# Performance work log

Hardware: AMD Instinct MI355X
Metric: run time of the kernel (lower is better)

Reference implementation:

```python
import jax, jax.numpy as jnp
import numpy as np

B, H0, W0, C = 8, 56, 56, 256
KC = VC = C
HID = 4 * C
NH = 8  # ChannelAttention default num_heads


def _ln(x, g, b, eps=1e-5):
    m = x.mean(-1, keepdims=True)
    v = jnp.var(x, axis=-1, keepdims=True)
    return (x - m) * jax.lax.rsqrt(v + eps) * g + b


def _dwconv(x, w, b, H, W):
    # x: [B, N, C] -> depthwise 3x3 on [B, C, H, W]
    Bn, N, Cc = x.shape
    t = x.transpose(0, 2, 1).reshape(Bn, Cc, H, W)
    y = jax.lax.conv_general_dilated(t, w, (1, 1), 'SAME', feature_group_count=Cc,
                                     dimension_numbers=('NCHW', 'OIHW', 'NCHW'))
    y = y + b[None, :, None, None]
    return y.reshape(Bn, Cc, H * W).transpose(0, 2, 1)


def _mixffn(x, H, W, w1, b1, dww, dwb, lg, lb, w2, b2):
    f = x @ w1.T + b1  # fc1(x), reused for the skip (torch computes it twice, same value)
    ax = jax.nn.gelu(_ln(_dwconv(f, dww, dwb, H, W) + f, lg, lb), approximate=False)
    return ax @ w2.T + b2


def _eff_attn(xn, kw, kb, qw, qb, vw, vb, rw, rb):
    # 1x1 convs == per-pixel linear; head_count=1
    k = jax.nn.softmax(xn @ kw.T + kb, axis=1)  # softmax over spatial N
    q = jax.nn.softmax(xn @ qw.T + qb, axis=2)  # softmax over key channels
    v = xn @ vw.T + vb
    ctx = jnp.einsum('bnk,bnv->bkv', k, v)      # [B, KC, VC]
    att = jnp.einsum('bkv,bnk->bnv', ctx, q)    # [B, N, VC]
    return att @ rw.T + rb


def _chan_attn(xn, temp, qkv_w, pw, pb):
    Bn, N, Cc = xn.shape
    d = Cc // NH
    qkv = (xn @ qkv_w.T).reshape(Bn, N, 3, NH, d).transpose(2, 0, 3, 4, 1)  # [3,B,h,d,N]
    q, k, v = qkv[0], qkv[1], qkv[2]
    q = q / jnp.maximum(jnp.linalg.norm(q, axis=-1, keepdims=True), 1e-12)
    k = k / jnp.maximum(jnp.linalg.norm(k, axis=-1, keepdims=True), 1e-12)
    attn = jax.nn.softmax(jnp.einsum('bhdn,bhen->bhde', q, k) * temp, axis=-1)  # [B,h,d,d]
    out = jnp.einsum('bhde,bhen->bhdn', attn, v).transpose(0, 3, 1, 2).reshape(Bn, N, Cc)
    return out @ pw.T + pb


def _forward(x, ln1g, ln1b, eakw, eakb, eaqw, eaqb, eavw, eavb, earw, earb,
             ln2g, ln2b, m1w1, m1b1, m1dww, m1dwb, m1lg, m1lb, m1w2, m1b2,
             ln3g, ln3b, catemp, caqkvw, capw, capb,
             ln4g, ln4b, m2w1, m2b1, m2dww, m2dwb, m2lg, m2lb, m2w2, m2b2, H, W):
    add1 = x + _eff_attn(_ln(x, ln1g, ln1b), eakw, eakb, eaqw, eaqb, eavw, eavb, earw, earb)
    add2 = add1 + _mixffn(_ln(add1, ln2g, ln2b), H, W, m1w1, m1b1, m1dww, m1dwb, m1lg, m1lb, m1w2, m1b2)
    add3 = add2 + _chan_attn(_ln(add2, ln3g, ln3b), catemp, caqkvw, capw, capb)
    return add3 + _mixffn(_ln(add3, ln4g, ln4b), H, W, m2w1, m2b1, m2dww, m2dwb, m2lg, m2lb, m2w2, m2b2)


def setup_inputs() -> dict:
    key = jax.random.key(0)
    ks = jax.random.split(key, 16)
    s = 0.02
    rn = lambda k, shape: jax.random.normal(k, shape, jnp.float32) * s
    f32 = jnp.float32
    return {
        'x': jax.random.normal(ks[0], (B, H0 * W0, C), f32),
        'H': H0, 'W': W0,
        'ln1g': jnp.ones(C, f32), 'ln1b': jnp.zeros(C, f32),
        'eakw': rn(ks[1], (KC, C)), 'eakb': jnp.zeros(KC, f32),
        'eaqw': rn(ks[2], (KC, C)), 'eaqb': jnp.zeros(KC, f32),
        'eavw': rn(ks[3], (VC, C)), 'eavb': jnp.zeros(VC, f32),
        'earw': rn(ks[4], (C, VC)), 'earb': jnp.zeros(C, f32),
        'ln2g': jnp.ones(C, f32), 'ln2b': jnp.zeros(C, f32),
        'm1w1': rn(ks[5], (HID, C)), 'm1b1': jnp.zeros(HID, f32),
        'm1dww': rn(ks[6], (HID, 1, 3, 3)), 'm1dwb': jnp.zeros(HID, f32),
        'm1lg': jnp.ones(HID, f32), 'm1lb': jnp.zeros(HID, f32),
        'm1w2': rn(ks[7], (C, HID)), 'm1b2': jnp.zeros(C, f32),
        'ln3g': jnp.ones(C, f32), 'ln3b': jnp.zeros(C, f32),
        'catemp': jnp.ones((NH, 1, 1), f32),
        'caqkvw': rn(ks[8], (3 * C, C)),
        'capw': rn(ks[9], (C, C)), 'capb': jnp.zeros(C, f32),
        'ln4g': jnp.ones(C, f32), 'ln4b': jnp.zeros(C, f32),
        'm2w1': rn(ks[10], (HID, C)), 'm2b1': jnp.zeros(HID, f32),
        'm2dww': rn(ks[11], (HID, 1, 3, 3)), 'm2dwb': jnp.zeros(HID, f32),
        'm2lg': jnp.ones(HID, f32), 'm2lb': jnp.zeros(HID, f32),
        'm2w2': rn(ks[12], (C, HID)), 'm2b2': jnp.zeros(C, f32),
    }


def reference(x, H, W, ln1g, ln1b, eakw, eakb, eaqw, eaqb, eavw, eavb, earw, earb,
              ln2g, ln2b, m1w1, m1b1, m1dww, m1dwb, m1lg, m1lb, m1w2, m1b2,
              ln3g, ln3b, catemp, caqkvw, capw, capb,
              ln4g, ln4b, m2w1, m2b1, m2dww, m2dwb, m2lg, m2lb, m2w2, m2b2):
    return _forward(x, ln1g, ln1b, eakw, eakb, eaqw, eaqb, eavw, eavb, earw, earb,
                    ln2g, ln2b, m1w1, m1b1, m1dww, m1dwb, m1lg, m1lb, m1w2, m1b2,
                    ln3g, ln3b, catemp, caqkvw, capw, capb,
                    ln4g, ln4b, m2w1, m2b1, m2dww, m2dwb, m2lg, m2lb, m2w2, m2b2, H, W)
```

## Files before the change

### kernel.cpp

```cpp
#include <hip/hip_runtime.h>
#include <hip/hip_bf16.h>

typedef __hip_bfloat16 bf16;
typedef __attribute__((ext_vector_type(8))) short short8;
typedef __attribute__((ext_vector_type(4))) float floatx4;

#define DI __device__ __forceinline__

DI float ldf(const float* p, long long i){ return p[i]; }
DI float ldf(const bf16* p, long long i){ return __bfloat162float(p[i]); }

DI unsigned short bfbits(float f){
    bf16 h = __float2bfloat16(f);
    return *reinterpret_cast<unsigned short*>(&h);
}
DI float bu(unsigned short u){
    union { unsigned int i; float f; } x; x.i = ((unsigned int)u) << 16; return x.f;
}

DI float gelu_exact(float x){
    float z = fabsf(x) * 0.70710678118654752f;
    float t = __builtin_amdgcn_rcpf(fmaf(0.3275911f, z, 1.f));
    float p = t * fmaf(t, fmaf(t, fmaf(t, fmaf(t, 1.061405429f, -1.453152027f),
                    1.421413741f), -0.284496736f), 0.254829592f);
    float e = __expf(-z*z);
    float er = fmaf(-p, e, 1.f);
    er = copysignf(er, x);
    return 0.5f * x * (1.f + er);
}

DI void gload16(const void* g, void* l){
    __builtin_amdgcn_global_load_lds(
        (const __attribute__((address_space(1))) unsigned int*)g,
        (__attribute__((address_space(3))) unsigned int*)l,
        16, 0, 0);
}

static constexpr int BATCH = 8;
static constexpr int HH = 56, WW = 56;
static constexpr int NPOS = HH * WW;
static constexpr int CDIM = 256;
static constexpr int HIDD = 1024;
static constexpr int MTOT = BATCH * NPOS;
static constexpr int NCHUNK = 49;
static constexpr int LP = 40;
static constexpr int TNS = 7;

struct WArgs {
    const float* src[10];
    bf16* dst[10];
    int n[10];
};
__global__ __launch_bounds__(256) void wcvt_kernel(WArgs a){
    int wid = blockIdx.y;
    int i = (blockIdx.x*256 + threadIdx.x) * 8;
    if (i >= a.n[wid]) return;
    const float* s = a.src[wid] + i;
    float4 f0 = *(const float4*)(s);
    float4 f1 = *(const float4*)(s + 4);
    union { uint4 u; unsigned short us[8]; } p;
    p.us[0]=bfbits(f0.x); p.us[1]=bfbits(f0.y); p.us[2]=bfbits(f0.z); p.us[3]=bfbits(f0.w);
    p.us[4]=bfbits(f1.x); p.us[5]=bfbits(f1.y); p.us[6]=bfbits(f1.z); p.us[7]=bfbits(f1.w);
    *(uint4*)(a.dst[wid] + i) = p.u;
}

__global__ __launch_bounds__(256) void wtrans_kernel(const float* __restrict__ w1, const float* __restrict__ w2,
                                                     float* __restrict__ t1, float* __restrict__ t2){
    int i = blockIdx.x*256 + threadIdx.x;
    const float* w = blockIdx.y ? w2 : w1;
    float* t = blockIdx.y ? t2 : t1;
    int tap = i >> 10, c = i & 1023;
    t[i] = w[c*9 + tap];
}

template<typename TC>
__global__ __launch_bounds__(256) void mfma_gemm(
    const bf16* __restrict__ A, const bf16* __restrict__ Bw,
    const float* __restrict__ bias, const float* __restrict__ addend,
    TC* __restrict__ C, int M, int N, int K, int lda,
    long long strA, long long strB, long long strC, long long strAdd)
{
    __shared__ __align__(16) float smemf[4608];
    short* As = (short*)smemf;
    short* Bs = (short*)smemf + 4096;
    int tid = threadIdx.x;
    int bz = blockIdx.z;
    A  += (long long)bz * strA;
    Bw += (long long)bz * strB;
    C  += (long long)bz * strC;
    if (addend) addend += (long long)bz * strAdd;

    int gx = gridDim.x;
    int nwg = gx * gridDim.y;
    int bidl = blockIdx.y * gx + blockIdx.x;
    int qq = nwg >> 3, rr = nwg & 7;
    int xcd = bidl & 7, ixx = bidl >> 3;
    int tile = (xcd < rr) ? (xcd*(qq+1) + ixx) : (rr*(qq+1) + (xcd-rr)*qq + ixx);
    int n0 = (tile % gx) * 128, m0 = (tile / gx) * 128;

    int w = tid >> 6, lane = tid & 63, lm = lane & 15, quad = lane >> 4;
    int mw = (w >> 1) * 64, nw = (w & 1) * 64;

    int c0 = w*128 + lane, c1 = c0 + 64;
    int ar0 = c0 >> 2, ac0 = (c0 & 3) ^ (ar0 & 3);
    int ar1 = c1 >> 2, ac1 = (c1 & 3) ^ (ar1 & 3);
    int rgA0 = m0 + ar0; if (rgA0 > M-1) rgA0 = M-1;
    int rgA1 = m0 + ar1; if (rgA1 > M-1) rgA1 = M-1;
    short* aL0 = &As[(2*w+0)*512];
    short* aL1 = &As[(2*w+1)*512];
    short* bL0 = &Bs[(2*w+0)*512];
    short* bL1 = &Bs[(2*w+1)*512];
    const bf16* Arow0 = A + (long long)rgA0*lda + ac0*8;
    const bf16* Arow1 = A + (long long)rgA1*lda + ac1*8;
    const bf16* Brow0 = Bw + (long long)(n0+ar0)*K + ac0*8;
    const bf16* Brow1 = Bw + (long long)(n0+ar1)*K + ac1*8;

    floatx4 z = {0.f, 0.f, 0.f, 0.f};
    floatx4 acc[4][4];
    #pragma unroll
    for (int mi = 0; mi < 4; mi++)
        #pragma unroll
        for (int ni = 0; ni < 4; ni++) acc[mi][ni] = z;

    int sq = quad ^ (lm & 3);

    for (int k0 = 0; k0 < K; k0 += 32){
        gload16(Arow0 + k0, aL0);
        gload16(Arow1 + k0, aL1);
        gload16(Brow0 + k0, bL0);
        gload16(Brow1 + k0, bL1);
        __syncthreads();
        short8 af[4], bfr[4];
        #pragma unroll
        for (int mi = 0; mi < 4; mi++)
            af[mi] = *(const short8*)&As[(((mw + mi*16 + lm)<<2) + sq)*8];
        #pragma unroll
        for (int ni = 0; ni < 4; ni++)
            bfr[ni] = *(const short8*)&Bs[(((nw + ni*16 + lm)<<2) + sq)*8];
        #pragma unroll
        for (int mi = 0; mi < 4; mi++)
            #pragma unroll
            for (int ni = 0; ni < 4; ni++)
                acc[mi][ni] = __builtin_amdgcn_mfma_f32_16x16x32_bf16(af[mi], bfr[ni], acc[mi][ni], 0, 0, 0);
        __syncthreads();
    }

    float bvv[4];
    #pragma unroll
    for (int ni = 0; ni < 4; ni++)
        bvv[ni] = bias ? bias[n0 + nw + ni*16 + lm] : 0.f;
    float* esc = smemf + w*1088;
    int rl0 = lane >> 3;
    #pragma unroll
    for (int mi = 0; mi < 4; mi++){
        #pragma unroll
        for (int ni = 0; ni < 4; ni++)
            #pragma unroll
            for (int r = 0; r < 4; r++)
                esc[(quad*4 + r)*68 + ni*16 + lm] = acc[mi][ni][r] + bvv[ni];
        #pragma unroll
        for (int p = 0; p < 2; p++){
            int rloc = p*8 + rl0;
            int rg = m0 + mw + mi*16 + rloc;
            if (rg < M){
                if constexpr (sizeof(TC) == 2){
                    int cl = (lane & 7) * 8;
                    float4 u0 = *(const float4*)&esc[rloc*68 + cl];
                    float4 u1 = *(const float4*)&esc[rloc*68 + cl + 4];
                    if (addend){
                        long long ai = (long long)rg*N + (n0 + nw + cl);
                        float4 a0 = *(const float4*)(addend + ai);
                        float4 a1 = *(const float4*)(addend + ai + 4);
                        u0.x+=a0.x; u0.y+=a0.y; u0.z+=a0.z; u0.w+=a0.w;
                        u1.x+=a1.x; u1.y+=a1.y; u1.z+=a1.z; u1.w+=a1.w;
                    }
                    union { uint4 u; unsigned short us[8]; } pk;
                    pk.us[0]=bfbits(u0.x); pk.us[1]=bfbits(u0.y); pk.us[2]=bfbits(u0.z); pk.us[3]=bfbits(u0.w);
                    pk.us[4]=bfbits(u1.x); pk.us[5]=bfbits(u1.y); pk.us[6]=bfbits(u1.z); pk.us[7]=bfbits(u1.w);
                    *(uint4*)(C + (long long)rg*N + (n0 + nw + cl)) = pk.u;
                } else {
                    int cl4 = (lane & 7) * 4;
                    long long co = (long long)rg*N + (n0 + nw);
                    float4 u0 = *(const float4*)&esc[rloc*68 + cl4];
                    float4 u1 = *(const float4*)&esc[rloc*68 + 32 + cl4];
                    if (addend){
                        float4 a0 = *(const float4*)(addend + co + cl4);
                        float4 a1 = *(const float4*)(addend + co + 32 + cl4);
                        u0.x+=a0.x; u0.y+=a0.y; u0.z+=a0.z; u0.w+=a0.w;
                        u1.x+=a1.x; u1.y+=a1.y; u1.z+=a1.z; u1.w+=a1.w;
                    }
                    *(float4*)(C + co + cl4) = u0;
                    *(float4*)(C + co + 32 + cl4) = u1;
                }
            }
        }
    }
}

__global__ __launch_bounds__(256) void gemm_tn_mfma(const bf16* __restrict__ V, const bf16* __restrict__ Kb,
                                                    float* __restrict__ part){
    __shared__ short As[128*LP];
    __shared__ short Bs[128*LP];
    int tid = threadIdx.x;
    int bz = blockIdx.z;
    int b = bz / TNS, s = bz % TNS;
    const bf16* Vb = V  + (long long)b*NPOS*CDIM;
    const bf16* Kc = Kb + (long long)b*NPOS*CDIM;
    int m0 = blockIdx.y * 128, n0 = blockIdx.x * 128;
    int w = tid >> 6, lane = tid & 63, lm = lane & 15, quad = lane >> 4;
    int mw = (w >> 1) * 64, nw = (w & 1) * 64;

    floatx4 z = {0.f,0.f,0.f,0.f};
    floatx4 acc[4][4];
    #pragma unroll
    for (int mi = 0; mi < 4; mi++)
        #pragma unroll
        for (int ni = 0; ni < 4; ni++) acc[mi][ni] = z;

    int r = tid & 31, cgrp = tid >> 5;

    for (int step = 0; step < 448/32; step++){
        int nb = s*448 + step*32;
        #pragma unroll
        for (int cc = 0; cc < 2; cc++){
            int ch = cgrp*8 + cc*64;
            short8 va = *(const short8*)(Vb + (long long)(nb + r)*CDIM + m0 + ch);
            short8 ka = *(const short8*)(Kc + (long long)(nb + r)*CDIM + n0 + ch);
            #pragma unroll
            for (int i = 0; i < 8; i++){
                As[(ch+i)*LP + r] = va[i];
                Bs[(ch+i)*LP + r] = ka[i];
            }
        }
        __syncthreads();
        short8 af[4], bfr[4];
        #pragma unroll
        for (int mi = 0; mi < 4; mi++)
            af[mi] = *(const short8*)&As[(mw + mi*16 + lm)*LP + quad*8];
        #pragma unroll
        for (int ni = 0; ni < 4; ni++)
            bfr[ni] = *(const short8*)&Bs[(nw + ni*16 + lm)*LP + quad*8];
        #pragma unroll
        for (int mi = 0; mi < 4; mi++)
            #pragma unroll
            for (int ni = 0; ni < 4; ni++)
                acc[mi][ni] = __builtin_amdgcn_mfma_f32_16x16x32_bf16(af[mi], bfr[ni], acc[mi][ni], 0, 0, 0);
        __syncthreads();
    }

    float* pb = part + (long long)bz * CDIM * CDIM;
    #pragma unroll
    for (int ni = 0; ni < 4; ni++){
        int cg = n0 + nw + ni*16 + lm;
        #pragma unroll
        for (int mi = 0; mi < 4; mi++){
            #pragma unroll
            for (int rr = 0; rr < 4; rr++){
                int rg = m0 + mw + mi*16 + quad*4 + rr;
                pb[(long long)rg*CDIM + cg] = acc[mi][ni][rr];
            }
        }
    }
}

__global__ __launch_bounds__(256) void ctx_reduce(const float* __restrict__ part, bf16* __restrict__ ctxb){
    long long idx = (long long)blockIdx.x*256 + threadIdx.x;
    int b = (int)(idx >> 16);
    int rem = (int)(idx & 65535);
    float s = 0.f;
    #pragma unroll
    for (int sp = 0; sp < TNS; sp++)
        s += part[((long long)(b*TNS+sp) << 16) + rem];
    ctxb[idx] = __float2bfloat16(s);
}

DI void st4o(float* p, long long i, float a, float b, float c, float d){
    float4 v = make_float4(a,b,c,d); *(float4*)(p + i) = v;
}
DI void st4o(bf16* p, long long i, float a, float b, float c, float d){
    union { unsigned long long u; unsigned short us[4]; } pk;
    pk.us[0]=bfbits(a); pk.us[1]=bfbits(b); pk.us[2]=bfbits(c); pk.us[3]=bfbits(d);
    *(unsigned long long*)(p + i) = pk.u;
}
template<typename TOUT>
__global__ __launch_bounds__(256) void ln4_kernel(const float* __restrict__ x, const float* __restrict__ g,
                                                  const float* __restrict__ b, TOUT* __restrict__ y){
    int wv = threadIdx.x >> 6, lane = threadIdx.x & 63;
    long long row = (long long)blockIdx.x*4 + wv;
    float4 v = *(const float4*)(x + row*256 + lane*4);
    float s  = v.x + v.y + v.z + v.w;
    float ss = v.x*v.x + v.y*v.y + v.z*v.z + v.w*v.w;
    #pragma unroll
    for (int off = 32; off > 0; off >>= 1){
        s  += __shfl_down(s,  off);
        ss += __shfl_down(ss, off);
    }
    s = __shfl(s, 0); ss = __shfl(ss, 0);
    float mean = s * (1.f/256.f);
    float var  = ss * (1.f/256.f) - mean*mean;
    float inv  = rsqrtf(var + 1e-5f);
    float4 gv = *(const float4*)(g + lane*4);
    float4 bv = *(const float4*)(b + lane*4);
    st4o(y, row*256 + lane*4,
         (v.x-mean)*inv*gv.x + bv.x, (v.y-mean)*inv*gv.y + bv.y,
         (v.z-mean)*inv*gv.z + bv.z, (v.w-mean)*inv*gv.w + bv.w);
}

__global__ __launch_bounds__(256) void colsm_p1(const float* __restrict__ x, float* __restrict__ lmax, float* __restrict__ lsum){
    int b = blockIdx.x / NCHUNK, ch = blockIdx.x % NCHUNK;
    int c = threadIdx.x;
    const float* base = x + ((long long)b*NPOS + ch*64)*512 + c;
    float m = -1e30f;
    for (int r = 0; r < 64; r++) m = fmaxf(m, base[(long long)r*512]);
    float s = 0.f;
    for (int r = 0; r < 64; r++) s += expf(base[(long long)r*512] - m);
    lmax[(long long)blockIdx.x*CDIM + c] = m;
    lsum[(long long)blockIdx.x*CDIM + c] = s;
}
__global__ __launch_bounds__(256) void colsm_p2(const float* __restrict__ lmax, const float* __restrict__ lsum,
                                                float* __restrict__ gmax, float* __restrict__ ginv){
    int b = blockIdx.x; int c = threadIdx.x;
    float g = -1e30f;
    for (int ch = 0; ch < NCHUNK; ch++) g = fmaxf(g, lmax[((long long)b*NCHUNK+ch)*CDIM + c]);
    float s = 0.f;
    for (int ch = 0; ch < NCHUNK; ch++)
        s += lsum[((long long)b*NCHUNK+ch)*CDIM + c] * expf(lmax[((long long)b*NCHUNK+ch)*CDIM + c] - g);
    gmax[b*CDIM + c] = g; ginv[b*CDIM + c] = 1.f / s;
}
__global__ __launch_bounds__(256) void colsm_p3(const float* __restrict__ x, bf16* __restrict__ y,
                                                const float* __restrict__ gmax, const float* __restrict__ ginv){
    long long idx = (long long)blockIdx.x*256 + threadIdx.x;
    int c = (int)(idx & 255);
    long long row = idx >> 8;
    int b = (int)(row / NPOS);
    y[idx] = __float2bfloat16(expf(x[row*512 + c] - gmax[b*CDIM + c]) * ginv[b*CDIM + c]);
}

__global__ __launch_bounds__(256) void rowsm4b_kernel(const float* __restrict__ x, const float* __restrict__ bias,
                                                      bf16* __restrict__ y){
    int wv = threadIdx.x >> 6, lane = threadIdx.x & 63;
    long long row = (long long)blockIdx.x*4 + wv;
    float4 v = *(const float4*)(x + row*512 + 256 + lane*4);
    float4 bb = *(const float4*)(bias + lane*4);
    v.x += bb.x; v.y += bb.y; v.z += bb.z; v.w += bb.w;
    float m = fmaxf(fmaxf(v.x, v.y), fmaxf(v.z, v.w));
    #pragma unroll
    for (int off = 32; off > 0; off >>= 1) m = fmaxf(m, __shfl_down(m, off));
    m = __shfl(m, 0);
    float e0 = expf(v.x - m), e1 = expf(v.y - m), e2 = expf(v.z - m), e3 = expf(v.w - m);
    float s = e0 + e1 + e2 + e3;
    #pragma unroll
    for (int off = 32; off > 0; off >>= 1) s += __shfl_down(s, off);
    s = __shfl(s, 0);
    float inv = 1.f / s;
    st4o(y, row*256 + lane*4, e0*inv, e1*inv, e2*inv, e3*inv);
}

__global__ __launch_bounds__(256) void dwconv_ln_gelu_kernel(const bf16* __restrict__ f, const float* __restrict__ wT,
        const float* __restrict__ db, const float* __restrict__ lg, const float* __restrict__ lb, bf16* __restrict__ out){
    __shared__ short Ls[18*1024];
    __shared__ float r1[2][2][128], r2[2][2][128];
    int tid = threadIdx.x;
    int b = blockIdx.x & 7;
    int rem = blockIdx.x >> 3;
    int h = rem / 14, w0 = (rem % 14) * 4;
    const bf16* fb = f + (long long)b * NPOS * HIDD;

    #pragma unroll
    for (int j = 0; j < 9; j++){
        int idx = j*256 + tid;
        int rc = idx >> 7, chunk = idx & 127;
        int row = rc / 6, col = rc % 6;
        int hy = h - 1 + row, wx = w0 - 1 + col;
        uint4 v = {0,0,0,0};
        if (hy >= 0 && hy < HH && wx >= 0 && wx < WW)
            v = *(const uint4*)(fb + (long long)(hy*WW + wx)*HIDD + chunk*8);
        *(uint4*)&Ls[rc*1024 + chunk*8] = v;
    }
    __syncthreads();

    int ph = tid >> 7, ct = tid & 127;
    int c0 = ct * 8;
    float sv[2][8];
    {
        float4 d0 = *(const float4*)(db + c0);
        float4 d1 = *(const float4*)(db + c0 + 4);
        #pragma unroll
        for (int pp = 0; pp < 2; pp++){
            sv[pp][0]=d0.x; sv[pp][1]=d0.y; sv[pp][2]=d0.z; sv[pp][3]=d0.w;
            sv[pp][4]=d1.x; sv[pp][5]=d1.y; sv[pp][6]=d1.z; sv[pp][7]=d1.w;
        }
    }
    #pragma unroll
    for (int tap = 0; tap < 9; tap++){
        int ky = tap / 3, kx = tap % 3;
        float4 w0v = *(const float4*)(wT + tap*1024 + c0);
        float4 w1v = *(const float4*)(wT + tap*1024 + c0 + 4);
        float wv[8] = {w0v.x,w0v.y,w0v.z,w0v.w,w1v.x,w1v.y,w1v.z,w1v.w};
        #pragma unroll
        for (int pp = 0; pp < 2; pp++){
            int pos_local = 2*ph + pp;
            short8 val = *(const short8*)&Ls[(ky*6 + pos_local + kx)*1024 + c0];
            #pragma unroll
            for (int i = 0; i < 8; i++){
                float fv = bu((unsigned short)val[i]);
                sv[pp][i] += fv * wv[i];
                if (tap == 4) sv[pp][i] += fv;
            }
        }
    }
    #pragma unroll
    for (int pp = 0; pp < 2; pp++){
        float s = 0.f, ss = 0.f;
        #pragma unroll
        for (int i = 0; i < 8; i++){ s += sv[pp][i]; ss += sv[pp][i]*sv[pp][i]; }
        r1[ph][pp][ct] = s; r2[ph][pp][ct] = ss;
    }
    __syncthreads();
    for (int st = 64; st > 0; st >>= 1){
        if (ct < st){
            #pragma unroll
            for (int pp = 0; pp < 2; pp++){
                r1[ph][pp][ct] += r1[ph][pp][ct+st];
                r2[ph][pp][ct] += r2[ph][pp][ct+st];
            }
        }
        __syncthreads();
    }
    float4 g0 = *(const float4*)(lg + c0), g1 = *(const float4*)(lg + c0 + 4);
    float4 b0 = *(const float4*)(lb + c0), b1 = *(const float4*)(lb + c0 + 4);
    float gg[8] = {g0.x,g0.y,g0.z,g0.w,g1.x,g1.y,g1.z,g1.w};
    float bb[8] = {b0.x,b0.y,b0.z,b0.w,b1.x,b1.y,b1.z,b1.w};
    #pragma unroll
    for (int pp = 0; pp < 2; pp++){
        int pos_local = 2*ph + pp;
        long long n = (long long)b*NPOS + h*WW + (w0 + pos_local);
        float mean = r1[ph][pp][0] * (1.f/HIDD);
        float var  = r2[ph][pp][0] * (1.f/HIDD) - mean*mean;
        float inv  = rsqrtf(var + 1e-5f);
        union { uint4 u; unsigned short us[8]; } ov;
        #pragma unroll
        for (int i = 0; i < 8; i++){
            float o = (sv[pp][i]-mean)*inv*gg[i] + bb[i];
            ov.us[i] = bfbits(gelu_exact(o));
        }
        *(uint4*)(out + n*HIDD + c0) = ov.u;
    }
}

__global__ __launch_bounds__(256) void ssq_p1(const bf16* __restrict__ qkv, float* __restrict__ lss){
    __shared__ float red[4][64][8];
    int b = blockIdx.x / NCHUNK, ch = blockIdx.x % NCHUNK;
    int tid = threadIdx.x;
    int col = (tid & 63) * 8;
    int rg = tid >> 6;
    float s[8] = {0,0,0,0,0,0,0,0};
    for (int r = rg*16; r < rg*16 + 16; r++){
        long long row = (long long)(b*NPOS + ch*64 + r);
        union { uint4 u; unsigned short us[8]; } v;
        v.u = *(const uint4*)(qkv + row*768 + col);
        #pragma unroll
        for (int i = 0; i < 8; i++){ float f = bu(v.us[i]); s[i] += f*f; }
    }
    #pragma unroll
    for (int i = 0; i < 8; i++) red[rg][tid & 63][i] = s[i];
    __syncthreads();
    if (tid < 64){
        #pragma unroll
        for (int i = 0; i < 8; i++){
            float t = red[0][tid][i] + red[1][tid][i] + red[2][tid][i] + red[3][tid][i];
            lss[(long long)blockIdx.x*512 + tid*8 + i] = t;
        }
    }
}
__global__ __launch_bounds__(256) void ssq_p2(const float* __restrict__ lss, float* __restrict__ invn){
    int b = blockIdx.x; int c = blockIdx.y*256 + threadIdx.x;
    float s = 0.f;
    for (int ch = 0; ch < NCHUNK; ch++) s += lss[((long long)b*NCHUNK+ch)*512 + c];
    invn[b*512 + c] = 1.f / fmaxf(sqrtf(s), 1e-12f);
}

__global__ __launch_bounds__(256) void chanattn_qk_part(const bf16* __restrict__ qkv, const float* __restrict__ invn,
                                                        float* __restrict__ part){
    __shared__ float qs[64][36];
    __shared__ float ks[64][36];
    int bz = blockIdx.x;
    int bh = bz / TNS, s = bz % TNS;
    int b = bh >> 3, hh = bh & 7;
    int tid = threadIdx.x;
    int d = tid >> 3, e0 = (tid & 7) * 4;
    int sr = tid >> 2, sc8 = (tid & 3) * 8;
    float invq[8], invk[8];
    {
        float4 a0 = *(const float4*)(invn + b*512 + hh*32 + sc8);
        float4 a1 = *(const float4*)(invn + b*512 + hh*32 + sc8 + 4);
        float4 b0 = *(const float4*)(invn + b*512 + 256 + hh*32 + sc8);
        float4 b1 = *(const float4*)(invn + b*512 + 256 + hh*32 + sc8 + 4);
        invq[0]=a0.x; invq[1]=a0.y; invq[2]=a0.z; invq[3]=a0.w;
        invq[4]=a1.x; invq[5]=a1.y; invq[6]=a1.z; invq[7]=a1.w;
        invk[0]=b0.x; invk[1]=b0.y; invk[2]=b0.z; invk[3]=b0.w;
        invk[4]=b1.x; invk[5]=b1.y; invk[6]=b1.z; invk[7]=b1.w;
    }
    float acc[4] = {0.f,0.f,0.f,0.f};
    for (int it = 0; it < 7; it++){
        int n0 = s*448 + it*64;
        {
            long long rowb = (long long)(b*NPOS + n0 + sr) * 768;
            union { uint4 u; unsigned short us[8]; } qv, kv;
            qv.u = *(const uint4*)(qkv + rowb + hh*32 + sc8);
            kv.u = *(const uint4*)(qkv + rowb + 256 + hh*32 + sc8);
            #pragma unroll
            for (int i = 0; i < 8; i++){
                qs[sr][sc8+i] = bu(qv.us[i]) * invq[i];
                ks[sr][sc8+i] = bu(kv.us[i]) * invk[i];
            }
        }
        __syncthreads();
        #pragma unroll 4
        for (int r = 0; r < 64; r++){
            float qv = qs[r][d];
            #pragma unroll
            for (int j = 0; j < 4; j++) acc[j] += qv * ks[r][e0+j];
        }
        __syncthreads();
    }
    #pragma unroll
    for (int j = 0; j < 4; j++)
        part[(long long)bz*1024 + d*32 + e0 + j] = acc[j];
}
__global__ __launch_bounds__(256) void chanattn_qk_fin(const float* __restrict__ part, const float* __restrict__ temp,
                                                       float* __restrict__ attn){
    __shared__ float att_s[32][33];
    int bh = blockIdx.x;
    int hh = bh & 7;
    int tid = threadIdx.x;
    int d = tid >> 3, e0 = (tid & 7) * 4;
    float t = temp[hh];
    #pragma unroll
    for (int j = 0; j < 4; j++){
        float s = 0.f;
        for (int sp = 0; sp < TNS; sp++)
            s += part[((long long)bh*TNS + sp)*1024 + d*32 + e0 + j];
        att_s[d][e0+j] = s * t;
    }
    __syncthreads();
    if (tid < 32){
        float m = -1e30f;
        for (int e = 0; e < 32; e++) m = fmaxf(m, att_s[tid][e]);
        float s = 0.f;
        for (int e = 0; e < 32; e++){ float ev = expf(att_s[tid][e] - m); att_s[tid][e] = ev; s += ev; }
        float inv = 1.f / s;
        for (int e = 0; e < 32; e++) att_s[tid][e] *= inv;
    }
    __syncthreads();
    #pragma unroll
    for (int j = 0; j < 4; j++)
        attn[(long long)bh*1024 + d*32 + e0 + j] = att_s[d][e0+j];
}

__global__ __launch_bounds__(256) void wcomb_kernel(const float* __restrict__ capw, const float* __restrict__ attn,
                                                    bf16* __restrict__ Wb){
    __shared__ float at_s[8192];
    int b = blockIdx.x, og = blockIdx.y;
    int tid = threadIdx.x;
    #pragma unroll
    for (int j = 0; j < 8; j++)
        *(float4*)&at_s[tid*32 + j*4] = *(const float4*)(attn + (long long)b*8192 + tid*32 + j*4);
    __syncthreads();
    int o = og*32 + (tid & 31);
    int h = tid >> 5;
    float acc[32];
    #pragma unroll
    for (int e = 0; e < 32; e++) acc[e] = 0.f;
    for (int d = 0; d < 32; d++){
        float w = capw[(long long)o*256 + h*32 + d];
        const float* ar = &at_s[h*1024 + d*32];
        #pragma unroll
        for (int eq = 0; eq < 8; eq++){
            float4 av = *(const float4*)(ar + eq*4);
            acc[eq*4+0] += w*av.x; acc[eq*4+1] += w*av.y;
            acc[eq*4+2] += w*av.z; acc[eq*4+3] += w*av.w;
        }
    }
    bf16* dst = Wb + (long long)b*65536 + (long long)o*256 + h*32;
    #pragma unroll
    for (int eq = 0; eq < 4; eq++){
        union { uint4 u; unsigned short us[8]; } p;
        #pragma unroll
        for (int i = 0; i < 8; i++) p.us[i] = bfbits(acc[eq*8+i]);
        *(uint4*)(dst + eq*8) = p.u;
    }
}

extern "C" void kernel_launch(void* const* d_in, const int* in_sizes, int n_in,
                              void* d_out, int out_size, void* d_ws, size_t ws_size,
                              hipStream_t stream){
    const float* x     = (const float*)d_in[0];
    const float* ln1g  = (const float*)d_in[3];
    const float* ln1b  = (const float*)d_in[4];
    const float* eakw  = (const float*)d_in[5];
    const float* eaqw  = (const float*)d_in[7];
    const float* eaqb  = (const float*)d_in[8];
    const float* eavw  = (const float*)d_in[9];
    const float* eavb  = (const float*)d_in[10];
    const float* earw  = (const float*)d_in[11];
    const float* earb  = (const float*)d_in[12];
    const float* ln2g  = (const float*)d_in[13];
    const float* ln2b  = (const float*)d_in[14];
    const float* m1w1  = (const float*)d_in[15];
    const float* m1b1  = (const float*)d_in[16];
    const float* m1dww = (const float*)d_in[17];
    const float* m1dwb = (const float*)d_in[18];
    const float* m1lg  = (const float*)d_in[19];
    const float* m1lb  = (const float*)d_in[20];
    const float* m1w2  = (const float*)d_in[21];
    const float* m1b2  = (const float*)d_in[22];
    const float* ln3g  = (const float*)d_in[23];
    const float* ln3b  = (const float*)d_in[24];
    const float* catemp= (const float*)d_in[25];
    const float* caqkvw= (const float*)d_in[26];
    const float* capw  = (const float*)d_in[27];
    const float* capb  = (const float*)d_in[28];
    const float* ln4g  = (const float*)d_in[29];
    const float* ln4b  = (const float*)d_in[30];
    const float* m2w1  = (const float*)d_in[31];
    const float* m2b1  = (const float*)d_in[32];
    const float* m2dww = (const float*)d_in[33];
    const float* m2dwb = (const float*)d_in[34];
    const float* m2lg  = (const float*)d_in[35];
    const float* m2lb  = (const float*)d_in[36];
    const float* m2w2  = (const float*)d_in[37];
    const float* m2b2  = (const float*)d_in[38];

    char* base = (char*)d_ws;
    auto alloc = [&](size_t nbytes){ char* p = base; base += (nbytes + 255) & ~(size_t)255; return p; };
    constexpr size_t SZ = (size_t)MTOT*CDIM*4;
    float* R  = (float*)alloc(SZ);
    float* A0 = (float*)alloc(SZ);
    float* A1 = (float*)alloc(SZ);
    float* B0 = (float*)alloc(SZ);
    float* B1 = (float*)alloc(SZ);
    bf16* A0b  = (bf16*)A0;
    bf16* kb   = (bf16*)A0;
    bf16* qb   = A0b + (size_t)MTOT*CDIM;
    bf16* vb   = (bf16*)A1;
    float* KQ  = B0;
    bf16* attb = (bf16*)B0;
    bf16* l2b  = (bf16*)A1;
    bf16* F    = (bf16*)B0;
    bf16* G    = (bf16*)A0;
    bf16* l3b  = (bf16*)B0;
    bf16* Qb   = (bf16*)A0;
    bf16* l4b  = (bf16*)A0;
    bf16* ctxb = (bf16*)alloc((size_t)BATCH*CDIM*CDIM*2);
    float* lmax = (float*)alloc((size_t)BATCH*NCHUNK*CDIM*4);
    float* lsum = (float*)alloc((size_t)BATCH*NCHUNK*CDIM*4);
    float* gmax = (float*)alloc((size_t)BATCH*CDIM*4);
    float* ginv = (float*)alloc((size_t)BATCH*CDIM*4);
    float* lss  = (float*)alloc((size_t)BATCH*NCHUNK*512*4);
    float* invn = (float*)alloc((size_t)BATCH*512*4);
    float* attnb= (float*)alloc((size_t)BATCH*8*32*32*4);
    float* ptn  = (float*)alloc((size_t)BATCH*TNS*CDIM*CDIM*4);
    float* pqk  = (float*)alloc((size_t)BATCH*8*TNS*1024*4);
    bf16* wbuf  = (bf16*)alloc((size_t)1572864*2);
    float* wT1  = (float*)alloc((size_t)9216*4);
    float* wT2  = (float*)alloc((size_t)9216*4);
    bf16* Wcb   = (bf16*)alloc((size_t)BATCH*CDIM*CDIM*2);

    bf16* kqw_b    = wbuf;
    bf16* eavw_b   = wbuf + 131072;
    bf16* earw_b   = wbuf + 196608;
    bf16* m1w1_b   = wbuf + 262144;
    bf16* m1w2_b   = wbuf + 524288;
    bf16* caqkvw_b = wbuf + 786432;
    bf16* m2w1_b   = wbuf + 1048576;
    bf16* m2w2_b   = wbuf + 1310720;

    dim3 blk(256);
    constexpr int MB = MTOT/128;
    long long sA1 = (long long)NPOS*CDIM;
    long long sB1 = (long long)CDIM*CDIM;

    {
        WArgs wa;
        const float* srcs[10] = {eakw, eaqw, eavw, earw, m1w1, m1w2, caqkvw, m2w1, m2w2, m2w2};
        bf16* dsts[10] = {kqw_b, kqw_b + 65536, eavw_b, earw_b, m1w1_b, m1w2_b, caqkvw_b, m2w1_b, m2w2_b, m2w2_b};
        int ns[10] = {65536, 65536, 65536, 65536, 262144, 262144, 196608, 262144, 262144, 0};
        for (int i = 0; i < 10; i++){ wa.src[i]=srcs[i]; wa.dst[i]=dsts[i]; wa.n[i]=ns[i]; }
        wcvt_kernel<<<dim3(128,10), blk, 0, stream>>>(wa);
        wtrans_kernel<<<dim3(36,2), blk, 0, stream>>>(m1dww, m2dww, wT1, wT2);
    }

    ln4_kernel<bf16><<<MTOT/4, blk, 0, stream>>>(x, ln1g, ln1b, A0b);
    mfma_gemm<float><<<dim3(4,MB,1), blk, 0, stream>>>(A0b, kqw_b, nullptr, nullptr, KQ, MTOT, 512, 256, 256, 0,0,0,0);
    mfma_gemm<bf16><<<dim3(2,MB,1), blk, 0, stream>>>(A0b, eavw_b, eavb, nullptr, vb, MTOT, 256, 256, 256, 0,0,0,0);
    rowsm4b_kernel<<<MTOT/4, blk, 0, stream>>>(KQ, eaqb, qb);
    colsm_p1<<<BATCH*NCHUNK, blk, 0, stream>>>(KQ, lmax, lsum);
    colsm_p2<<<BATCH, blk, 0, stream>>>(lmax, lsum, gmax, ginv);
    colsm_p3<<<MTOT, blk, 0, stream>>>(KQ, kb, gmax, ginv);
    gemm_tn_mfma<<<dim3(2,2,BATCH*TNS), blk, 0, stream>>>(vb, kb, ptn);
    ctx_reduce<<<(BATCH*65536)/256, blk, 0, stream>>>(ptn, ctxb);
    mfma_gemm<bf16><<<dim3(2,25,BATCH), blk, 0, stream>>>(qb, ctxb, nullptr, nullptr, attb,
            NPOS, 256, 256, 256, sA1, sB1, sA1, 0);
    mfma_gemm<float><<<dim3(2,MB,1), blk, 0, stream>>>(attb, earw_b, earb, x, R, MTOT, 256, 256, 256, 0,0,0,0);

    ln4_kernel<bf16><<<MTOT/4, blk, 0, stream>>>(R, ln2g, ln2b, l2b);
    mfma_gemm<bf16><<<dim3(8,MB,1), blk, 0, stream>>>(l2b, m1w1_b, m1b1, nullptr, F, MTOT, 1024, 256, 256, 0,0,0,0);
    dwconv_ln_gelu_kernel<<<BATCH*HH*14, blk, 0, stream>>>(F, wT1, m1dwb, m1lg, m1lb, G);
    mfma_gemm<float><<<dim3(2,MB,1), blk, 0, stream>>>(G, m1w2_b, m1b2, R, R, MTOT, 256, 1024, 1024, 0,0,0,0);

    ln4_kernel<bf16><<<MTOT/4, blk, 0, stream>>>(R, ln3g, ln3b, l3b);
    mfma_gemm<bf16><<<dim3(6,MB,1), blk, 0, stream>>>(l3b, caqkvw_b, nullptr, nullptr, Qb, MTOT, 768, 256, 256, 0,0,0,0);
    ssq_p1<<<BATCH*NCHUNK, blk, 0, stream>>>(Qb, lss);
    ssq_p2<<<dim3(BATCH,2), blk, 0, stream>>>(lss, invn);
    chanattn_qk_part<<<BATCH*8*TNS, blk, 0, stream>>>(Qb, invn, pqk);
    chanattn_qk_fin<<<BATCH*8, blk, 0, stream>>>(pqk, catemp, attnb);
    wcomb_kernel<<<dim3(BATCH,8), blk, 0, stream>>>(capw, attnb, Wcb);
    mfma_gemm<float><<<dim3(2,25,BATCH), blk, 0, stream>>>(Qb + 512, Wcb, capb, R, R,
            NPOS, 256, 256, 768, (long long)NPOS*768, sB1, sA1, sA1);

    ln4_kernel<bf16><<<MTOT/4, blk, 0, stream>>>(R, ln4g, ln4b, l4b);
    mfma_gemm<bf16><<<dim3(8,MB,1), blk, 0, stream>>>(l4b, m2w1_b, m2b1, nullptr, F, MTOT, 1024, 256, 256, 0,0,0,0);
    dwconv_ln_gelu_kernel<<<BATCH*HH*14, blk, 0, stream>>>(F, wT2, m2dwb, m2lg, m2lb, G);
    mfma_gemm<float><<<dim3(2,MB,1), blk, 0, stream>>>(G, m2w2_b, m2b2, R, (float*)d_out, MTOT, 256, 1024, 1024, 0,0,0,0);
}
```

Measured before the change: 600.6 us.

## Double-buffer GEMM LDS tiles and use wave-shuffle LayerNorm reduction in dwconv

The MFMA GEMM now keeps two LDS stages and issues global-to-LDS loads for the next K-slice before computing on the current one, so memory latency can overlap with MFMA work. LDS use grows from about 18KB to 32KB per block, which may lower occupancy. The dwconv+LN+GELU kernel replaces its log-step shared-memory tree reduction, which needed a barrier at every step, with a single LDS pass followed by wave shuffles, and reuses the input tile buffer for the partial sums.

```diff
diff --git a/kernel.cpp b/kernel.cpp
--- a/kernel.cpp
+++ b/kernel.cpp
@@ -6,9 +6,6 @@
 typedef __attribute__((ext_vector_type(4))) float floatx4;
 
 #define DI __device__ __forceinline__
-
-DI float ldf(const float* p, long long i){ return p[i]; }
-DI float ldf(const bf16* p, long long i){ return __bfloat162float(p[i]); }
 
 DI unsigned short bfbits(float f){
     bf16 h = __float2bfloat16(f);
@@ -80,9 +77,8 @@
     TC* __restrict__ C, int M, int N, int K, int lda,
     long long strA, long long strB, long long strC, long long strAdd)
 {
-    __shared__ __align__(16) float smemf[4608];
-    short* As = (short*)smemf;
-    short* Bs = (short*)smemf + 4096;
+    __shared__ __align__(16) float smemf[8192];
+    short* S = (short*)smemf;
     int tid = threadIdx.x;
     int bz = blockIdx.z;
     A  += (long long)bz * strA;
@@ -106,10 +102,10 @@
     int ar1 = c1 >> 2, ac1 = (c1 & 3) ^ (ar1 & 3);
     int rgA0 = m0 + ar0; if (rgA0 > M-1) rgA0 = M-1;
     int rgA1 = m0 + ar1; if (rgA1 > M-1) rgA1 = M-1;
-    short* aL0 = &As[(2*w+0)*512];
-    short* aL1 = &As[(2*w+1)*512];
-    short* bL0 = &Bs[(2*w+0)*512];
-    short* bL1 = &Bs[(2*w+1)*512];
+    short* aL0 = S + (2*w+0)*512;
+    short* aL1 = S + (2*w+1)*512;
+    short* bL0 = S + 4096 + (2*w+0)*512;
+    short* bL1 = S + 4096 + (2*w+1)*512;
     const bf16* Arow0 = A + (long long)rgA0*lda + ac0*8;
     const bf16* Arow1 = A + (long long)rgA1*lda + ac1*8;
     const bf16* Brow0 = Bw + (long long)(n0+ar0)*K + ac0*8;
@@ -124,19 +120,26 @@
 
     int sq = quad ^ (lm & 3);
 
-    for (int k0 = 0; k0 < K; k0 += 32){
-        gload16(Arow0 + k0, aL0);
-        gload16(Arow1 + k0, aL1);
-        gload16(Brow0 + k0, bL0);
-        gload16(Brow1 + k0, bL1);
-        __syncthreads();
+    auto STAGE = [&](int k0, int poff){
+        gload16(Arow0 + k0, aL0 + poff);
+        gload16(Arow1 + k0, aL1 + poff);
+        gload16(Brow0 + k0, bL0 + poff);
+        gload16(Brow1 + k0, bL1 + poff);
+    };
+
+    STAGE(0, 0);
+    __syncthreads();
+    int NS = K >> 5;
+    for (int st = 0; st < NS; st++){
+        int poff = (st & 1) << 13;
+        if (st + 1 < NS) STAGE((st+1)*32, poff ^ 8192);
         short8 af[4], bfr[4];
         #pragma unroll
         for (int mi = 0; mi < 4; mi++)
-            af[mi] = *(const short8*)&As[(((mw + mi*16 + lm)<<2) + sq)*8];
+            af[mi] = *(const short8*)&S[poff + (((mw + mi*16 + lm)<<2) + sq)*8];
         #pragma unroll
         for (int ni = 0; ni < 4; ni++)
-            bfr[ni] = *(const short8*)&Bs[(((nw + ni*16 + lm)<<2) + sq)*8];
+            bfr[ni] = *(const short8*)&S[poff + 4096 + (((nw + ni*16 + lm)<<2) + sq)*8];
         #pragma unroll
         for (int mi = 0; mi < 4; mi++)
             #pragma unroll
@@ -359,7 +362,6 @@
 __global__ __launch_bounds__(256) void dwconv_ln_gelu_kernel(const bf16* __restrict__ f, const float* __restrict__ wT,
         const float* __restrict__ db, const float* __restrict__ lg, const float* __restrict__ lb, bf16* __restrict__ out){
     __shared__ short Ls[18*1024];
-    __shared__ float r1[2][2][128], r2[2][2][128];
     int tid = threadIdx.x;
     int b = blockIdx.x & 7;
     int rem = blockIdx.x >> 3;
@@ -409,24 +411,29 @@
             }
         }
     }
+    float* rr = (float*)Ls;
+    __syncthreads();
     #pragma unroll
     for (int pp = 0; pp < 2; pp++){
         float s = 0.f, ss = 0.f;
         #pragma unroll
         for (int i = 0; i < 8; i++){ s += sv[pp][i]; ss += sv[pp][i]*sv[pp][i]; }
-        r1[ph][pp][ct] = s; r2[ph][pp][ct] = ss;
-    }
-    __syncthreads();
-    for (int st = 64; st > 0; st >>= 1){
-        if (ct < st){
-            #pragma unroll
-            for (int pp = 0; pp < 2; pp++){
-                r1[ph][pp][ct] += r1[ph][pp][ct+st];
-                r2[ph][pp][ct] += r2[ph][pp][ct+st];
-            }
-        }
-        __syncthreads();
-    }
+        rr[(ph*2+pp)*128 + ct] = s;
+        rr[512 + (ph*2+pp)*128 + ct] = ss;
+    }
+    __syncthreads();
+    {
+        int wv = tid >> 6, ln = tid & 63;
+        float s  = rr[wv*128 + ln]       + rr[wv*128 + ln + 64];
+        float ss = rr[512 + wv*128 + ln] + rr[512 + wv*128 + ln + 64];
+        #pragma unroll
+        for (int off = 32; off > 0; off >>= 1){
+            s  += __shfl_down(s,  off);
+            ss += __shfl_down(ss, off);
+        }
+        if (ln == 0){ rr[1024 + wv] = s; rr[1028 + wv] = ss; }
+    }
+    __syncthreads();
     float4 g0 = *(const float4*)(lg + c0), g1 = *(const float4*)(lg + c0 + 4);
     float4 b0 = *(const float4*)(lb + c0), b1 = *(const float4*)(lb + c0 + 4);
     float gg[8] = {g0.x,g0.y,g0.z,g0.w,g1.x,g1.y,g1.z,g1.w};
@@ -435,8 +442,8 @@
     for (int pp = 0; pp < 2; pp++){
         int pos_local = 2*ph + pp;
         long long n = (long long)b*NPOS + h*WW + (w0 + pos_local);
-        float mean = r1[ph][pp][0] * (1.f/HIDD);
-        float var  = r2[ph][pp][0] * (1.f/HIDD) - mean*mean;
+        float mean = rr[1024 + ph*2+pp] * (1.f/HIDD);
+        float var  = rr[1028 + ph*2+pp] * (1.f/HIDD) - mean*mean;
         float inv  = rsqrtf(var + 1e-5f);
         union { uint4 u; unsigned short us[8]; } ov;
         #pragma unroll
```

Result: faster. 566.0 us (-5.8%).
